# Performance work log

Measured on AMD Instinct MI355X. Metric: run time of the kernel, lower is better.

Reference implementation:

```python
import jax, jax.numpy as jnp
import numpy as np

LN_EPS = 1e-5
ATTN_EPS = 1e-6
NHEAD = 8

def layer_norm(x, g, b):
    m = jnp.mean(x, axis=-1, keepdims=True)
    v = jnp.var(x, axis=-1, keepdims=True)
    return (x - m) * jax.lax.rsqrt(v + LN_EPS) * g + b

def rope_maps(H, W, D):
    # 2D RoPE over the head dim: even freq-pairs encode row position i, odd pairs col position j.
    quarter = D // 4
    div = jnp.exp(jnp.arange(quarter, dtype=jnp.float32) * (-np.log(10000.0) / quarter))
    ang_i = jnp.arange(1, H + 1, dtype=jnp.float32)[:, None, None] * div  # [H,1,q]
    ang_j = jnp.arange(1, W + 1, dtype=jnp.float32)[None, :, None] * div  # [1,W,q]
    ang_i = jnp.broadcast_to(ang_i, (H, W, quarter))
    ang_j = jnp.broadcast_to(ang_j, (H, W, quarter))
    sin_h = jnp.stack((jnp.sin(ang_i), jnp.sin(ang_j)), axis=-1).reshape(H, W, D // 2)
    cos_h = jnp.stack((jnp.cos(ang_i), jnp.cos(ang_j)), axis=-1).reshape(H, W, D // 2)
    # repeat_interleave(2) to act on (x_{2i}, x_{2i+1}) rotation pairs
    return jnp.repeat(sin_h, 2, axis=-1), jnp.repeat(cos_h, 2, axis=-1)  # each [H,W,D]

def rotate_half(x):
    xp = x.reshape(*x.shape[:-1], -1, 2)
    x1, x2 = xp[..., 0], xp[..., 1]
    return jnp.stack((-x2, x1), axis=-1).reshape(x.shape)

def apply_rope(x, sin, cos, H, W):
    # x: [N, L, nh, D] with L = H*W
    N, L, nh, D = x.shape
    xg = x.reshape(N, H, W, nh, D)
    s = sin[None, :, :, None, :]
    c = cos[None, :, :, None, :]
    out = xg * c + rotate_half(xg) * s
    return out.reshape(N, L, nh, D)

def rope_linear_attention(q, k, v, H, W):
    # elu+1 feature map linear attention (LoFTR) with 2D RoPE on Q/K
    Q = jax.nn.elu(q) + 1.0
    K = jax.nn.elu(k) + 1.0
    v_len = v.shape[1]
    v = v / v_len  # prevent overflow, restored at the end
    sin, cos = rope_maps(H, W, Q.shape[-1])
    Q = apply_rope(Q, sin, cos, H, W)
    K = apply_rope(K, sin, cos, H, W)
    KV = jnp.einsum('nshd,nshv->nhdv', K, v)                       # [N,nh,D,D]
    Z = 1.0 / (jnp.einsum('nlhd,nhd->nlh', Q, K.sum(axis=1)) + ATTN_EPS)
    return jnp.einsum('nlhd,nhdv,nlh->nlhv', Q, KV, Z) * v_len     # [N,L,nh,D]

def setup_inputs() -> dict:
    key = jax.random.key(0)
    ks = jax.random.split(key, 8)
    N, L, C = 4, 16384, 256
    s = 0.02
    return {
        'x': jax.random.normal(ks[0], (N, L, C), jnp.float32),
        'source': jax.random.normal(ks[1], (N, L, C), jnp.float32),
        'Wq': jax.random.normal(ks[2], (C, C), jnp.float32) * s,
        'Wk': jax.random.normal(ks[3], (C, C), jnp.float32) * s,
        'Wv': jax.random.normal(ks[4], (C, C), jnp.float32) * s,
        'Wm': jax.random.normal(ks[5], (C, C), jnp.float32) * s,
        'W1': jax.random.normal(ks[6], (2 * C, 2 * C), jnp.float32) * s,
        'W2': jax.random.normal(ks[7], (C, 2 * C), jnp.float32) * s,
        'ln1_g': jnp.ones((C,), jnp.float32),
        'ln1_b': jnp.zeros((C,), jnp.float32),
        'ln2_g': jnp.ones((C,), jnp.float32),
        'ln2_b': jnp.zeros((C,), jnp.float32),
        'H': 128,
        'W': 128,
    }

def reference(x, source, Wq, Wk, Wv, Wm, W1, W2, ln1_g, ln1_b, ln2_g, ln2_b, H, W):
    N, L, C = x.shape
    D = C // NHEAD
    q = (x @ Wq.T).reshape(N, L, NHEAD, D)
    k = (source @ Wk.T).reshape(N, L, NHEAD, D)
    v = (source @ Wv.T).reshape(N, L, NHEAD, D)
    msg = rope_linear_attention(q, k, v, H, W).reshape(N, L, C)
    msg = layer_norm(msg @ Wm.T, ln1_g, ln1_b)
    h = jnp.concatenate([x, msg], axis=-1)              # [N,L,2C]
    h = jax.nn.relu(h @ W1.T) @ W2.T                    # [N,L,C]
    msg = layer_norm(h, ln2_g, ln2_b)
    return x + msg
```

## Files before the change

kernel.cpp:

```cpp
#include <hip/hip_runtime.h>
#include <hip/hip_bf16.h>
#include <math.h>

#define NB 4
#define LL 16384
#define CC 256
#define NHD 8
#define DH 32
#define MROWS (NB*LL)

typedef __hip_bfloat16 bf16;
typedef __attribute__((ext_vector_type(8))) short short8;
typedef __attribute__((ext_vector_type(4))) float floatx4;

__device__ __forceinline__ float u2f(unsigned short u) {
  return __uint_as_float(((unsigned)u) << 16);
}
__device__ __forceinline__ unsigned short f2u(float f) {
  bf16 t = __float2bfloat16(f);
  unsigned short u;
  __builtin_memcpy(&u, &t, 2);
  return u;
}

__global__ __launch_bounds__(256) void convert_kernel(
    const float* __restrict__ in, bf16* __restrict__ out, int n8)
{
  int i = blockIdx.x*256 + threadIdx.x;
  if (i >= n8) return;
  const float4* p = (const float4*)in + (size_t)i*2;
  float4 f0 = p[0], f1 = p[1];
  unsigned short t[8] = {f2u(f0.x),f2u(f0.y),f2u(f0.z),f2u(f0.w),
                         f2u(f1.x),f2u(f1.y),f2u(f1.z),f2u(f1.w)};
  *(uint4*)(out + (size_t)i*8) = *(uint4*)t;
}

__global__ __launch_bounds__(256) void convert_weights_kernel(
    const float* __restrict__ Wq, const float* __restrict__ Wk,
    const float* __restrict__ Wv, const float* __restrict__ Wm,
    const float* __restrict__ W1, const float* __restrict__ W2,
    bf16* __restrict__ dst)
{
  int i = blockIdx.x*256 + threadIdx.x;
  const float* src; int off8;
  if      (i < 8192)  { src = Wq; off8 = i; }
  else if (i < 16384) { src = Wk; off8 = i-8192; }
  else if (i < 24576) { src = Wv; off8 = i-16384; }
  else if (i < 32768) { src = Wm; off8 = i-24576; }
  else if (i < 65536) { src = W1; off8 = i-32768; }
  else                { src = W2; off8 = i-65536; }
  const float4* p = (const float4*)src + (size_t)off8*2;
  float4 f0 = p[0], f1 = p[1];
  unsigned short t[8] = {f2u(f0.x),f2u(f0.y),f2u(f0.z),f2u(f0.w),
                         f2u(f1.x),f2u(f1.y),f2u(f1.z),f2u(f1.w)};
  *(uint4*)(dst + (size_t)i*8) = *(uint4*)t;
}

template<int EPI>
__global__ __launch_bounds__(256) void gemm_m97(
    const bf16* __restrict__ A0, int K0, const bf16* __restrict__ A1,
    const bf16* __restrict__ B, bf16* __restrict__ C,
    int M, int N, int K)
{
  __shared__ __align__(16) unsigned short As[128*32];
  __shared__ __align__(16) unsigned short Bs[128*32];
  const int tid  = threadIdx.x;
  const int lane = tid & 63, wave = tid >> 6;
  const int wm = wave & 1, wn = wave >> 1;
  const int l15 = lane & 15, quad = lane >> 4;

  const int nbn = N >> 7;
  const int sh  = (nbn == 2) ? 4 : 5;
  const int w   = blockIdx.x & ((1 << sh) - 1);
  const int g   = blockIdx.x >> sh;
  const int bm  = g*8 + (w & 7);
  const int bn  = w >> 3;

  const int srow  = tid >> 2;
  const int skcol = (tid & 3) << 3;

  floatx4 acc[4][4] = {};

  for (int kt = 0; kt < K; kt += 32) {
    const bf16* aSrc; int lda, kof;
    if (kt < K0) { aSrc = A0; lda = K0;     kof = kt; }
    else         { aSrc = A1; lda = K - K0; kof = kt - K0; }
    #pragma unroll
    for (int c = 0; c < 2; c++) {
      const bf16* gp = aSrc + (size_t)(bm*128 + c*64 + srow)*lda + kof + skcol;
      __builtin_amdgcn_global_load_lds(
          (const __attribute__((address_space(1))) void*)gp,
          (__attribute__((address_space(3))) void*)(As + c*2048 + tid*8),
          16, 0, 0);
    }
    #pragma unroll
    for (int c = 0; c < 2; c++) {
      const bf16* gp = B + (size_t)(bn*128 + c*64 + srow)*K + kt + skcol;
      __builtin_amdgcn_global_load_lds(
          (const __attribute__((address_space(1))) void*)gp,
          (__attribute__((address_space(3))) void*)(Bs + c*2048 + tid*8),
          16, 0, 0);
    }
    __syncthreads();
    short8 a[4], b[4];
    #pragma unroll
    for (int i = 0; i < 4; i++) {
      a[i] = *(const short8*)&As[(wm*64 + i*16 + l15)*32 + quad*8];
      b[i] = *(const short8*)&Bs[(wn*64 + i*16 + l15)*32 + quad*8];
    }
    #pragma unroll
    for (int i = 0; i < 4; i++)
      #pragma unroll
      for (int j = 0; j < 4; j++)
        acc[i][j] = __builtin_amdgcn_mfma_f32_16x16x32_bf16(a[i], b[j], acc[i][j], 0, 0, 0);
    __syncthreads();
  }

  const int row0 = bm*128 + wm*64 + quad*4;
  const int col0 = bn*128 + wn*64 + l15;
  if (EPI == 2) {
    const int pp_e = l15 >> 1;
    const int pp_o = pp_e + 8;
    const int par  = pp_e & 1;
    const float dv_e = __expf(-1.15129254650564f * (float)(pp_e >> 1));
    const float dv_o = __expf(-1.15129254650564f * (float)(pp_o >> 1));
    const float sgn = (l15 & 1) ? 1.f : -1.f;
    #pragma unroll
    for (int i = 0; i < 4; i++) {
      #pragma unroll
      for (int r = 0; r < 4; r++) {
        int row = row0 + i*16 + r;
        int l = row & (LL-1);
        float pos = par ? (float)((l & 127) + 1) : (float)((l >> 7) + 1);
        float ae = pos * dv_e, ao = pos * dv_o;
        float se = __sinf(ae), ce = __cosf(ae);
        float so = __sinf(ao), co = __cosf(ao);
        #pragma unroll
        for (int j = 0; j < 4; j++) {
          float s = (j & 1) ? so : se;
          float c = (j & 1) ? co : ce;
          float v = acc[i][j][r];
          v = v > 0.f ? v + 1.f : __expf(v);
          float p = __shfl_xor(v, 1, 64);
          float o = fmaf(v, c, sgn * p * s);
          C[(size_t)row*N + (col0 + j*16)] = __float2bfloat16(o);
        }
      }
    }
  } else {
    #pragma unroll
    for (int i = 0; i < 4; i++)
      #pragma unroll
      for (int j = 0; j < 4; j++)
        #pragma unroll
        for (int r = 0; r < 4; r++) {
          float v = acc[i][j][r];
          if (EPI == 1) v = fmaxf(v, 0.f);
          C[(size_t)(row0 + i*16 + r)*N + (col0 + j*16)] = __float2bfloat16(v);
        }
  }
}

__global__ __launch_bounds__(256) void zero_kernel(float* __restrict__ p, int n)
{
  int i = blockIdx.x*256 + threadIdx.x;
  if (i < n) p[i] = 0.f;
}

__global__ __launch_bounds__(256) void kv_kernel(
    const bf16* __restrict__ Kr, const bf16* __restrict__ V,
    float* __restrict__ KV, float* __restrict__ Ksum)
{
  __shared__ __align__(16) float Ks[64][32];
  __shared__ __align__(16) float Vs[64][32];
  const int nh = blockIdx.x;
  const int n = nh >> 3, h = nh & 7;
  const int s0 = blockIdx.y * 1024;
  const int tid = threadIdx.x;
  const int d = tid >> 3, e0 = (tid & 7) << 2;
  float acc[4] = {0.f,0.f,0.f,0.f};
  float ksl = 0.f;
  for (int sub = 0; sub < 1024; sub += 64) {
    #pragma unroll
    for (int i = 0; i < 4; i++) {
      int flat = (tid + i*256) << 1;
      int sl = flat >> 5, dd = flat & 31;
      size_t g = (((size_t)(n*LL + s0 + sub + sl) * NHD + h) << 5) + dd;
      ushort2 uk = *(const ushort2*)(Kr + g);
      ushort2 uv = *(const ushort2*)(V + g);
      Ks[sl][dd]   = u2f(uk.x); Ks[sl][dd+1] = u2f(uk.y);
      Vs[sl][dd]   = u2f(uv.x); Vs[sl][dd+1] = u2f(uv.y);
    }
    __syncthreads();
    #pragma unroll 8
    for (int ss = 0; ss < 64; ss++) {
      float kd = Ks[ss][d];
      float4 v4 = *(const float4*)&Vs[ss][e0];
      acc[0] = fmaf(kd, v4.x, acc[0]);
      acc[1] = fmaf(kd, v4.y, acc[1]);
      acc[2] = fmaf(kd, v4.z, acc[2]);
      acc[3] = fmaf(kd, v4.w, acc[3]);
    }
    if (tid < 32) {
      #pragma unroll 8
      for (int ss = 0; ss < 64; ss++) ksl += Ks[ss][tid];
    }
    __syncthreads();
  }
  float* kvp = KV + ((size_t)nh << 10) + (d << 5) + e0;
  atomicAdd(kvp+0, acc[0]); atomicAdd(kvp+1, acc[1]);
  atomicAdd(kvp+2, acc[2]); atomicAdd(kvp+3, acc[3]);
  if (tid < 32) atomicAdd(Ksum + (nh << 5) + tid, ksl);
}

__global__ __launch_bounds__(256) void attn_out_kernel(
    const bf16* __restrict__ Qr, const float* __restrict__ KV,
    const float* __restrict__ Ksum, bf16* __restrict__ Out)
{
  __shared__ float KVs[8192];
  __shared__ float Kss[256];
  __shared__ float Qs[16][256];
  const int blk = blockIdx.x;
  const int n = blk >> 10;
  const int tid = threadIdx.x;
  const size_t rowBase = (size_t)blk * 16;
  for (int i = tid; i < 8192; i += 256) KVs[i] = KV[((size_t)n << 13) + i];
  Kss[tid] = Ksum[(n << 8) + tid];
  for (int i = tid; i < 4096; i += 256) ((float*)Qs)[i] = u2f(*(const unsigned short*)(Qr + (rowBase << 8) + i));
  __syncthreads();
  const int h = tid >> 5, e = tid & 31;
  const float* kvh = &KVs[(h << 10) + e];
  const float* ksh = &Kss[h << 5];
  for (int r = 0; r < 16; r++) {
    const float* qh = &Qs[r][h << 5];
    float denom = 1e-6f;
    float num = 0.f;
    #pragma unroll
    for (int d = 0; d < 32; d++) {
      float qd = qh[d];
      denom = fmaf(qd, ksh[d], denom);
      num   = fmaf(qd, kvh[d << 5], num);
    }
    Out[((rowBase + r) << 8) + tid] = __float2bfloat16(num / denom);
  }
}

__global__ __launch_bounds__(256) void ln_kernel(
    const bf16* __restrict__ X, const float* __restrict__ g, const float* __restrict__ b,
    bf16* __restrict__ Out)
{
  __shared__ float ps[4], psq[4], stat[2];
  int row = blockIdx.x, tid = threadIdx.x;
  float v = __bfloat162float(X[((size_t)row << 8) + tid]);
  float s = v, sq = v*v;
  #pragma unroll
  for (int o = 32; o > 0; o >>= 1) {
    s  += __shfl_down(s, o, 64);
    sq += __shfl_down(sq, o, 64);
  }
  if ((tid & 63) == 0) { ps[tid>>6] = s; psq[tid>>6] = sq; }
  __syncthreads();
  if (tid == 0) {
    float S = ps[0]+ps[1]+ps[2]+ps[3];
    float SQ = psq[0]+psq[1]+psq[2]+psq[3];
    float mean = S * (1.f/256.f);
    float var = SQ * (1.f/256.f) - mean*mean;
    stat[0] = mean; stat[1] = rsqrtf(var + 1e-5f);
  }
  __syncthreads();
  float mean = stat[0], rstd = stat[1];
  Out[((size_t)row << 8) + tid] = __float2bfloat16(
      (v - mean)*rstd*g[tid] + b[tid]);
}

__global__ __launch_bounds__(256) void ln_add_kernel(
    const bf16* __restrict__ X, const float* __restrict__ g, const float* __restrict__ b,
    const float* __restrict__ xin, float* __restrict__ Out)
{
  __shared__ float ps[4], psq[4], stat[2];
  int row = blockIdx.x, tid = threadIdx.x;
  size_t idx = ((size_t)row << 8) + tid;
  float v = __bfloat162float(X[idx]);
  float s = v, sq = v*v;
  #pragma unroll
  for (int o = 32; o > 0; o >>= 1) {
    s  += __shfl_down(s, o, 64);
    sq += __shfl_down(sq, o, 64);
  }
  if ((tid & 63) == 0) { ps[tid>>6] = s; psq[tid>>6] = sq; }
  __syncthreads();
  if (tid == 0) {
    float S = ps[0]+ps[1]+ps[2]+ps[3];
    float SQ = psq[0]+psq[1]+psq[2]+psq[3];
    float mean = S * (1.f/256.f);
    float var = SQ * (1.f/256.f) - mean*mean;
    stat[0] = mean; stat[1] = rsqrtf(var + 1e-5f);
  }
  __syncthreads();
  float mean = stat[0], rstd = stat[1];
  float lnv = (v - mean)*rstd*g[tid] + b[tid];
  Out[idx] = xin[idx] + lnv;
}

extern "C" void kernel_launch(void* const* d_in, const int* in_sizes, int n_in,
                              void* d_out, int out_size, void* d_ws, size_t ws_size,
                              hipStream_t stream) {
  const float* x   = (const float*)d_in[0];
  const float* src = (const float*)d_in[1];
  const float* Wq  = (const float*)d_in[2];
  const float* Wk  = (const float*)d_in[3];
  const float* Wv  = (const float*)d_in[4];
  const float* Wm  = (const float*)d_in[5];
  const float* W1  = (const float*)d_in[6];
  const float* W2  = (const float*)d_in[7];
  const float* g1  = (const float*)d_in[8];
  const float* b1  = (const float*)d_in[9];
  const float* g2  = (const float*)d_in[10];
  const float* b2  = (const float*)d_in[11];
  float* out = (float*)d_out;

  bf16* ws = (bf16*)d_ws;
  const size_t BUFH = (size_t)MROWS * CC;
  bf16* R0 = ws;
  bf16* R1 = ws + BUFH;
  bf16* R2 = ws + 2*BUFH;
  bf16* R3 = ws + 3*BUFH;
  bf16* WB = ws + 4*BUFH;
  bf16* wq = WB, *wk = WB+65536, *wv = WB+131072, *wm = WB+196608,
      *w1 = WB+262144, *w2 = WB+524288;
  float* KV   = (float*)(WB + 655360);
  float* Ksum = KV + NB*NHD*DH*DH;

  dim3 blk(256);
  const int n8 = MROWS*CC/8;
  convert_kernel<<<(n8+255)/256, blk, 0, stream>>>(x,   R0, n8);
  convert_kernel<<<(n8+255)/256, blk, 0, stream>>>(src, R1, n8);
  convert_weights_kernel<<<320, blk, 0, stream>>>(Wq, Wk, Wv, Wm, W1, W2, WB);

  const int G256 = (MROWS/128)*(CC/128);
  const int G512 = (MROWS/128)*(2*CC/128);
  gemm_m97<2><<<G256, blk, 0, stream>>>(R1, CC, nullptr, wk, R2, MROWS, CC, CC);
  gemm_m97<0><<<G256, blk, 0, stream>>>(R1, CC, nullptr, wv, R3, MROWS, CC, CC);
  int kvN = NB*NHD*DH*DH + NB*NHD*DH;
  zero_kernel<<<(kvN+255)/256, blk, 0, stream>>>(KV, kvN);
  kv_kernel<<<dim3(NB*NHD, 16), blk, 0, stream>>>(R2, R3, KV, Ksum);
  gemm_m97<2><<<G256, blk, 0, stream>>>(R0, CC, nullptr, wq, R1, MROWS, CC, CC);
  attn_out_kernel<<<MROWS/16, blk, 0, stream>>>(R1, KV, Ksum, R2);
  gemm_m97<0><<<G256, blk, 0, stream>>>(R2, CC, nullptr, wm, R3, MROWS, CC, CC);
  ln_kernel<<<MROWS, blk, 0, stream>>>(R3, g1, b1, R3);
  gemm_m97<1><<<G512, blk, 0, stream>>>(R0, CC, R3, w1, R1, MROWS, 2*CC, 2*CC);
  gemm_m97<0><<<G256, blk, 0, stream>>>(nullptr, 0, R1, w2, R3, MROWS, CC, 2*CC);
  ln_add_kernel<<<MROWS, blk, 0, stream>>>(R3, g2, b2, x, out);
}
```

Measured before the change: 572.8 us.

## Split KV reduction across more blocks with direct global-to-LDS loads; vectorize Q load

The KV/Ksum reduction kernel now launches 128 blocks per (batch, head) instead of 16. Each block loads one 128-row K/V tile directly into LDS as raw bf16 using global_load_lds, with no per-element conversion and no inner sync loop. The attention-output kernel now reads Q with 16-byte vector loads instead of scalar bf16 loads. This trades a short serial loop in few blocks for far more parallelism, at the cost of roughly eight times more atomicAdds into the small KV buffer.

```diff
diff --git a/kernel.cpp b/kernel.cpp
--- a/kernel.cpp
+++ b/kernel.cpp
@@ -171,46 +171,50 @@
     const bf16* __restrict__ Kr, const bf16* __restrict__ V,
     float* __restrict__ KV, float* __restrict__ Ksum)
 {
-  __shared__ __align__(16) float Ks[64][32];
-  __shared__ __align__(16) float Vs[64][32];
+  __shared__ __align__(16) unsigned short Ks[128*32];
+  __shared__ __align__(16) unsigned short Vs[128*32];
   const int nh = blockIdx.x;
   const int n = nh >> 3, h = nh & 7;
-  const int s0 = blockIdx.y * 1024;
+  const int s0 = blockIdx.y * 128;
   const int tid = threadIdx.x;
+
+  #pragma unroll
+  for (int c = 0; c < 2; c++) {
+    int row = c*64 + (tid >> 2);
+    int d0  = (tid & 3) << 3;
+    size_t g = (((size_t)(n*LL + s0 + row) * NHD + h) << 5) + d0;
+    __builtin_amdgcn_global_load_lds(
+        (const __attribute__((address_space(1))) void*)(Kr + g),
+        (__attribute__((address_space(3))) void*)(Ks + c*2048 + tid*8),
+        16, 0, 0);
+    __builtin_amdgcn_global_load_lds(
+        (const __attribute__((address_space(1))) void*)(V + g),
+        (__attribute__((address_space(3))) void*)(Vs + c*2048 + tid*8),
+        16, 0, 0);
+  }
+  __syncthreads();
+
   const int d = tid >> 3, e0 = (tid & 7) << 2;
-  float acc[4] = {0.f,0.f,0.f,0.f};
-  float ksl = 0.f;
-  for (int sub = 0; sub < 1024; sub += 64) {
-    #pragma unroll
-    for (int i = 0; i < 4; i++) {
-      int flat = (tid + i*256) << 1;
-      int sl = flat >> 5, dd = flat & 31;
-      size_t g = (((size_t)(n*LL + s0 + sub + sl) * NHD + h) << 5) + dd;
-      ushort2 uk = *(const ushort2*)(Kr + g);
-      ushort2 uv = *(const ushort2*)(V + g);
-      Ks[sl][dd]   = u2f(uk.x); Ks[sl][dd+1] = u2f(uk.y);
-      Vs[sl][dd]   = u2f(uv.x); Vs[sl][dd+1] = u2f(uv.y);
-    }
-    __syncthreads();
+  float acc0 = 0.f, acc1 = 0.f, acc2 = 0.f, acc3 = 0.f;
+  #pragma unroll 8
+  for (int ss = 0; ss < 128; ss++) {
+    float kd = u2f(Ks[ss*32 + d]);
+    ushort4 v4 = *(const ushort4*)&Vs[ss*32 + e0];
+    acc0 = fmaf(kd, u2f(v4.x), acc0);
+    acc1 = fmaf(kd, u2f(v4.y), acc1);
+    acc2 = fmaf(kd, u2f(v4.z), acc2);
+    acc3 = fmaf(kd, u2f(v4.w), acc3);
+  }
+  float* kvp = KV + ((size_t)nh << 10) + (d << 5) + e0;
+  atomicAdd(kvp+0, acc0); atomicAdd(kvp+1, acc1);
+  atomicAdd(kvp+2, acc2); atomicAdd(kvp+3, acc3);
+
+  if (tid < 32) {
+    float ksl = 0.f;
     #pragma unroll 8
-    for (int ss = 0; ss < 64; ss++) {
-      float kd = Ks[ss][d];
-      float4 v4 = *(const float4*)&Vs[ss][e0];
-      acc[0] = fmaf(kd, v4.x, acc[0]);
-      acc[1] = fmaf(kd, v4.y, acc[1]);
-      acc[2] = fmaf(kd, v4.z, acc[2]);
-      acc[3] = fmaf(kd, v4.w, acc[3]);
-    }
-    if (tid < 32) {
-      #pragma unroll 8
-      for (int ss = 0; ss < 64; ss++) ksl += Ks[ss][tid];
-    }
-    __syncthreads();
-  }
-  float* kvp = KV + ((size_t)nh << 10) + (d << 5) + e0;
-  atomicAdd(kvp+0, acc[0]); atomicAdd(kvp+1, acc[1]);
-  atomicAdd(kvp+2, acc[2]); atomicAdd(kvp+3, acc[3]);
-  if (tid < 32) atomicAdd(Ksum + (nh << 5) + tid, ksl);
+    for (int ss = 0; ss < 128; ss++) ksl += u2f(Ks[ss*32 + tid]);
+    atomicAdd(Ksum + (nh << 5) + tid, ksl);
+  }
 }
 
 __global__ __launch_bounds__(256) void attn_out_kernel(
@@ -226,7 +230,14 @@
   const size_t rowBase = (size_t)blk * 16;
   for (int i = tid; i < 8192; i += 256) KVs[i] = KV[((size_t)n << 13) + i];
   Kss[tid] = Ksum[(n << 8) + tid];
-  for (int i = tid; i < 4096; i += 256) ((float*)Qs)[i] = u2f(*(const unsigned short*)(Qr + (rowBase << 8) + i));
+  #pragma unroll
+  for (int it = 0; it < 2; it++) {
+    int i = it*256 + tid;
+    short8 u = *(const short8*)(Qr + (rowBase << 8) + (size_t)i*8);
+    float* qp = ((float*)Qs) + (size_t)i*8;
+    #pragma unroll
+    for (int j = 0; j < 8; j++) qp[j] = u2f((unsigned short)u[j]);
+  }
   __syncthreads();
   const int h = tid >> 5, e = tid & 31;
   const float* kvh = &KVs[(h << 10) + e];
@@ -343,7 +354,7 @@
   gemm_m97<0><<<G256, blk, 0, stream>>>(R1, CC, nullptr, wv, R3, MROWS, CC, CC);
   int kvN = NB*NHD*DH*DH + NB*NHD*DH;
   zero_kernel<<<(kvN+255)/256, blk, 0, stream>>>(KV, kvN);
-  kv_kernel<<<dim3(NB*NHD, 16), blk, 0, stream>>>(R2, R3, KV, Ksum);
+  kv_kernel<<<dim3(NB*NHD, 128), blk, 0, stream>>>(R2, R3, KV, Ksum);
   gemm_m97<2><<<G256, blk, 0, stream>>>(R0, CC, nullptr, wq, R1, MROWS, CC, CC);
   attn_out_kernel<<<MROWS/16, blk, 0, stream>>>(R1, KV, Ksum, R2);
   gemm_m97<0><<<G256, blk, 0, stream>>>(R2, CC, nullptr, wm, R3, MROWS, CC, CC);
```

Measured after the change: 599.9 us. 1.05x slower.
